# Optimization experiments

Measured on AMD Instinct MI355X. Metric: run time of the kernel, lower is better.

The kernel has to match this reference:

```python
import jax, jax.numpy as jnp
import numpy as np

D, H, E, K, N, PROJ = 512, 1024, 8, 2, 65536, 256
C = N * K // E  # expert capacity (capacity_factor=1.0 over the full token count)
LOG100 = float(np.log(100.0))


def _l2norm(v, axis=-1):
    return v / (jnp.linalg.norm(v, axis=axis, keepdims=True) + 1e-12)


def _moe(x, mask, Wp, bp, sim, temp, W1, b1, W2, b2):
    # tutel 'cosine_top' gate: cosine sim between projected tokens and expert embeddings,
    # scaled by clamped learned temperature.
    logits = _l2norm(x @ Wp + bp) @ _l2norm(sim, axis=0)
    logits = logits * jnp.exp(jnp.minimum(temp, LOG100))
    gates_all = jax.nn.softmax(logits, axis=-1)
    g, idx = jax.lax.top_k(gates_all, K)                      # [N,K]
    g = g / (jnp.sum(g, axis=-1, keepdims=True) + 1e-9)       # normalize top-k gates
    g = g * mask[:, None]                                     # zero out tokens not in this domain
    e = idx.reshape(-1)                                       # [N*K] expert id per slot
    gflat = g.reshape(-1)
    valid = jnp.repeat(mask, K)                               # [N*K]
    oh = jax.nn.one_hot(e, E, dtype=jnp.float32) * valid[:, None]
    pos = (jnp.cumsum(oh, axis=0) * oh).sum(-1).astype(jnp.int32) - 1  # slot within expert
    keep = ((pos >= 0) & (pos < C)).astype(x.dtype)           # drop overflow / masked tokens
    posc = jnp.clip(pos, 0, C - 1)
    tok = jnp.arange(N * K, dtype=jnp.int32) // K
    # dispatch -> [E,C,D]
    xd = jnp.zeros((E, C, D), x.dtype).at[e, posc].add(x[tok] * keep[:, None])
    # grouped expert FFN
    h = jax.nn.relu(jnp.einsum('ecd,edh->ech', xd, W1) + b1[:, None, :])
    y = jnp.einsum('ech,ehd->ecd', h, W2) + b2[:, None, :]
    # combine back to tokens
    out = jnp.zeros((N, D), x.dtype).at[tok].add(y[e, posc] * (gflat * keep)[:, None])
    return out


def _make_params(key):
    ks = jax.random.split(key, 4)
    Wp = jax.random.normal(ks[0], (D, PROJ), jnp.float32) * 0.02
    bp = jnp.zeros((PROJ,), jnp.float32)
    sim = jax.random.normal(ks[1], (PROJ, E), jnp.float32) * 0.02
    temp = jnp.asarray(np.log(10.0), jnp.float32)
    W1 = jax.random.normal(ks[2], (E, D, H), jnp.float32) * (1.0 / np.sqrt(D))
    b1 = jnp.zeros((E, H), jnp.float32)
    W2 = jax.random.normal(ks[3], (E, H, D), jnp.float32) * (1.0 / np.sqrt(H))
    b2 = jnp.zeros((E, D), jnp.float32)
    return Wp, bp, sim, temp, W1, b1, W2, b2


def setup_inputs():
    key = jax.random.key(0)
    kx, kl, k1, k2, k3, ksc = jax.random.split(key, 6)
    inp = {
        'x': jax.random.normal(kx, (N, D), jnp.float32),
        'domain_label': jax.random.randint(kl, (N,), 0, 2),
        'domain_scale': jax.random.normal(ksc, (1,), jnp.float32) * 0.1,
    }
    for name, k in (('sh', k1), ('day', k2), ('nt', k3)):
        Wp, bp, sim, temp, W1, b1, W2, b2 = _make_params(k)
        inp.update({name + '_Wp': Wp, name + '_bp': bp, name + '_sim': sim, name + '_temp': temp,
                    name + '_W1': W1, name + '_b1': b1, name + '_W2': W2, name + '_b2': b2})
    return inp


def reference(x, domain_label, domain_scale,
              sh_Wp, sh_bp, sh_sim, sh_temp, sh_W1, sh_b1, sh_W2, sh_b2,
              day_Wp, day_bp, day_sim, day_temp, day_W1, day_b1, day_W2, day_b2,
              nt_Wp, nt_bp, nt_sim, nt_temp, nt_W1, nt_b1, nt_W2, nt_b2):
    ones = jnp.ones((N,), jnp.float32)
    day = (domain_label == 0).astype(jnp.float32)
    night = (domain_label == 1).astype(jnp.float32)
    f_shared = _moe(x, ones, sh_Wp, sh_bp, sh_sim, sh_temp, sh_W1, sh_b1, sh_W2, sh_b2)
    f_domain = (_moe(x, day, day_Wp, day_bp, day_sim, day_temp, day_W1, day_b1, day_W2, day_b2)
                + _moe(x, night, nt_Wp, nt_bp, nt_sim, nt_temp, nt_W1, nt_b1, nt_W2, nt_b2))
    return f_shared + domain_scale * f_domain
```

## Files before the change

kernel.cpp:

```cpp
#include <hip/hip_runtime.h>

#define NTOK 65536
#define DDIM 512
#define HDIM 1024
#define NEXP 8
#define PROJ 256
#define CAP  16384
#define NSLOT (2*NTOK)
#define LOG100 4.605170185988091f

typedef __attribute__((ext_vector_type(8))) short bf16x8;
typedef __attribute__((ext_vector_type(4))) short short4v;
typedef __attribute__((ext_vector_type(4))) float f32x4;

__device__ inline float bf2f(unsigned short u){
    union { float f; unsigned int i; } c; c.i = ((unsigned int)u) << 16; return c.f;
}
__device__ inline unsigned short f2bf(float f){
    union { float f; unsigned int i; } c; c.f = f;
    unsigned int x = c.i;
    return (unsigned short)((x + 0x7fffu + ((x >> 16) & 1u)) >> 16);
}
__device__ inline void gload16(const void* g, void* lds){
    __builtin_amdgcn_global_load_lds(
        (const __attribute__((address_space(1))) unsigned int*)g,
        (__attribute__((address_space(3))) unsigned int*)lds, 16, 0, 0);
}

__global__ void init_k(const float4* __restrict__ x, ushort4* __restrict__ xb,
                       float4* __restrict__ out){
    long i = (long)blockIdx.x * 256 + threadIdx.x;
    float4 f = x[i];
    ushort4 u; u.x = f2bf(f.x); u.y = f2bf(f.y); u.z = f2bf(f.z); u.w = f2bf(f.w);
    xb[i] = u;
    out[i] = float4{0.f, 0.f, 0.f, 0.f};
}

__device__ inline void trans_body(const float* in, unsigned short* out, int R, int C){
    int rbase = blockIdx.y * 32, cbase = blockIdx.x * 32;
    if (rbase >= R || cbase >= C) return;
    __shared__ float tile[32][33];
    int tx = threadIdx.x, ty = threadIdx.y;
    #pragma unroll
    for (int i = 0; i < 4; i++)
        tile[ty + i*8][tx] = in[(long)(rbase + ty + i*8) * C + cbase + tx];
    __syncthreads();
    #pragma unroll
    for (int i = 0; i < 4; i++)
        out[(long)(cbase + ty + i*8) * R + rbase + tx] = f2bf(tile[tx][ty + i*8]);
}

__global__ __launch_bounds__(256)
void trans2_k(const float* __restrict__ W1, const float* __restrict__ W2,
              unsigned short* __restrict__ W1T, unsigned short* __restrict__ W2T)
{
    int z = blockIdx.z;
    if (z < 8) trans_body(W1 + (size_t)z*DDIM*HDIM, W1T + (size_t)z*DDIM*HDIM, DDIM, HDIM);
    else       trans_body(W2 + (size_t)(z-8)*DDIM*HDIM, W2T + (size_t)(z-8)*DDIM*HDIM, HDIM, DDIM);
}

struct W12P { const float* W1[3]; const float* W2[3]; };
__global__ __launch_bounds__(256)
void transW12all_k(W12P wp, unsigned short* __restrict__ W1T3, unsigned short* __restrict__ W2T3)
{
    int z = blockIdx.z, m = z >> 4, piece = z & 15;
    if (piece < 8)
        trans_body(wp.W1[m] + (size_t)piece*DDIM*HDIM,
                   W1T3 + ((size_t)m*8 + piece)*DDIM*HDIM, DDIM, HDIM);
    else
        trans_body(wp.W2[m] + (size_t)(piece-8)*DDIM*HDIM,
                   W2T3 + ((size_t)m*8 + piece-8)*DDIM*HDIM, HDIM, DDIM);
}

struct TpArgs { const float* Wp[3]; };
__global__ __launch_bounds__(256)
void transWp_k(TpArgs ta, unsigned short* __restrict__ WpT3)
{
    int m = blockIdx.z;
    trans_body(ta.Wp[m], WpT3 + (size_t)m*PROJ*DDIM, DDIM, PROJ);
}

struct SimArgs { const float* sim[3]; };
__global__ void simn3_k(SimArgs sa, float* __restrict__ simn3){
    __shared__ float red[256];
    const float* sim = sa.sim[blockIdx.x];
    float* simn = simn3 + (size_t)blockIdx.x * PROJ * NEXP;
    int j = threadIdx.x;
    for (int e = 0; e < NEXP; e++){
        float v = sim[j*NEXP + e];
        red[j] = v*v;
        __syncthreads();
        for (int s = 128; s > 0; s >>= 1){
            if (j < s) red[j] += red[j + s];
            __syncthreads();
        }
        float nrm = sqrtf(red[0]) + 1e-12f;
        __syncthreads();
        simn[j*NEXP + e] = v / nrm;
    }
}

struct WprodArgs { const float* Wp[3]; const float* bp[3]; };
__global__ __launch_bounds__(256)
void wprod_k(WprodArgs wa, const float* __restrict__ simn3,
             float* __restrict__ Wn3, float* __restrict__ bd3)
{
    int m = blockIdx.x;
    __shared__ float Sn[PROJ*NEXP];
    const float* Wp = wa.Wp[m];
    int t = threadIdx.x;
    for (int i = t; i < PROJ*NEXP; i += 256) Sn[i] = simn3[(size_t)m*PROJ*NEXP + i];
    __syncthreads();
    for (int r = t; r < DDIM; r += 256){
        float d[8];
        #pragma unroll
        for (int e = 0; e < 8; e++) d[e] = 0.f;
        for (int p = 0; p < PROJ; p++){
            float w = Wp[(size_t)r*PROJ + p];
            #pragma unroll
            for (int e = 0; e < 8; e++) d[e] = fmaf(w, Sn[p*8+e], d[e]);
        }
        #pragma unroll
        for (int e = 0; e < 8; e++) Wn3[((size_t)m*DDIM + r)*8 + e] = d[e];
    }
    if (t < 8){
        float s = 0.f;
        for (int p = 0; p < PROJ; p++) s = fmaf(wa.bp[m][p], Sn[p*8+t], s);
        bd3[m*8 + t] = s;
    }
}

struct PssArgs { const float* bp[3]; };
__global__ __launch_bounds__(256)
void pss_k(const unsigned short* __restrict__ WpT3, const unsigned short* __restrict__ xb,
           PssArgs pa, float* __restrict__ ssbuf)
{
    __shared__ __align__(16) short As[128*32];
    __shared__ __align__(16) short Bs[128*32];
    __shared__ float ssl[2][128];
    const int m = blockIdx.z;
    const int row0 = blockIdx.x * 128;
    const int n0 = blockIdx.y * 128;
    const unsigned short* AT = WpT3 + (size_t)m * PROJ * DDIM;
    const float* bp = pa.bp[m];

    const int t = threadIdx.x, w = t >> 6, l = t & 63;
    const int qrow = l >> 2, kc = (l & 3) * 8;
    long arowg[2], browg[2];
    #pragma unroll
    for (int q = 0; q < 2; q++){
        arowg[q] = (long)(row0 + w*32 + q*16 + qrow) * DDIM;
        browg[q] = (long)(n0   + w*32 + q*16 + qrow) * DDIM;
    }
    const int wm = (w >> 1) * 64, wn = (w & 1) * 64;
    const int fr = l & 15, fk = l >> 4;
    const int koff = fk * 8, fk4 = fk * 4;

    f32x4 acc[4][4];
    #pragma unroll
    for (int i = 0; i < 4; i++)
        #pragma unroll
        for (int j = 0; j < 4; j++) acc[i][j] = (f32x4){0.f, 0.f, 0.f, 0.f};

    for (int k0 = 0; k0 < DDIM; k0 += 32){
        __syncthreads();
        #pragma unroll
        for (int q = 0; q < 2; q++) gload16(AT + arowg[q] + k0 + kc, As + w*1024 + q*512);
        #pragma unroll
        for (int q = 0; q < 2; q++) gload16(xb + browg[q] + k0 + kc, Bs + w*1024 + q*512);
        __syncthreads();
        bf16x8 af[4], bfv[4];
        #pragma unroll
        for (int i = 0; i < 4; i++) af[i]  = *(const bf16x8*)&As[(wm + i*16 + fr)*32 + koff];
        #pragma unroll
        for (int j = 0; j < 4; j++) bfv[j] = *(const bf16x8*)&Bs[(wn + j*16 + fr)*32 + koff];
        #pragma unroll
        for (int i = 0; i < 4; i++)
            #pragma unroll
            for (int j = 0; j < 4; j++)
                acc[i][j] = __builtin_amdgcn_mfma_f32_16x16x32_bf16(af[i], bfv[j], acc[i][j], 0, 0, 0);
    }

    float part[4];
    #pragma unroll
    for (int j = 0; j < 4; j++){
        float s = 0.f;
        #pragma unroll
        for (int i = 0; i < 4; i++){
            int mc = row0 + wm + i*16 + fk4;
            float4 bb = *(const float4*)(bp + mc);
            float v0 = acc[i][j][0] + bb.x;
            float v1 = acc[i][j][1] + bb.y;
            float v2 = acc[i][j][2] + bb.z;
            float v3 = acc[i][j][3] + bb.w;
            s += v0*v0 + v1*v1 + v2*v2 + v3*v3;
        }
        s += __shfl_xor(s, 16, 64);
        s += __shfl_xor(s, 32, 64);
        part[j] = s;
    }
    if (fk == 0){
        #pragma unroll
        for (int j = 0; j < 4; j++) ssl[w >> 1][wn + j*16 + fr] = part[j];
    }
    __syncthreads();
    if (t < 128)
        ssbuf[((size_t)blockIdx.x*3 + m)*NTOK + n0 + t] = ssl[0][t] + ssl[1][t];
}

struct GfArgs { const float* tp[3]; };
__global__ __launch_bounds__(256)
void gatefin3_k(const float* __restrict__ x, const int* __restrict__ label,
                const float* __restrict__ Wn3, const float* __restrict__ bd3,
                const float* __restrict__ ssbuf, GfArgs gf,
                int* __restrict__ idx3, float* __restrict__ gw3)
{
    __shared__ float pd[3][64][26];
    const int t = threadIdx.x;
    const int tok = t & 63;
    const int qu = __builtin_amdgcn_readfirstlane(t >> 6);
    const int n = blockIdx.x * 64 + tok;

    float dots[3][8];
    #pragma unroll
    for (int m = 0; m < 3; m++)
        #pragma unroll
        for (int e = 0; e < 8; e++) dots[m][e] = 0.f;

    const float4* xp = (const float4*)(x + (size_t)n * DDIM + qu * 128);
    for (int c = 0; c < 8; c++){
        float4 xv[4];
        #pragma unroll
        for (int u = 0; u < 4; u++) xv[u] = xp[c*4 + u];
        #pragma unroll
        for (int kk = 0; kk < 16; kk++){
            float a = (kk & 2) ? ((kk & 1) ? xv[kk>>2].w : xv[kk>>2].z)
                               : ((kk & 1) ? xv[kk>>2].y : xv[kk>>2].x);
            int k = qu*128 + c*16 + kk;
            #pragma unroll
            for (int m = 0; m < 3; m++){
                const float* wr = Wn3 + ((size_t)m*DDIM + k)*8;
                float4 w0 = *(const float4*)wr;
                float4 w1 = *(const float4*)(wr + 4);
                dots[m][0] = fmaf(a, w0.x, dots[m][0]);
                dots[m][1] = fmaf(a, w0.y, dots[m][1]);
                dots[m][2] = fmaf(a, w0.z, dots[m][2]);
                dots[m][3] = fmaf(a, w0.w, dots[m][3]);
                dots[m][4] = fmaf(a, w1.x, dots[m][4]);
                dots[m][5] = fmaf(a, w1.y, dots[m][5]);
                dots[m][6] = fmaf(a, w1.z, dots[m][6]);
                dots[m][7] = fmaf(a, w1.w, dots[m][7]);
            }
        }
    }
    if (qu != 0){
        #pragma unroll
        for (int m = 0; m < 3; m++)
            #pragma unroll
            for (int e = 0; e < 8; e++) pd[qu-1][tok][m*8+e] = dots[m][e];
    }
    __syncthreads();
    if (qu == 0){
        #pragma unroll
        for (int qq = 0; qq < 3; qq++)
            #pragma unroll
            for (int m = 0; m < 3; m++)
                #pragma unroll
                for (int e = 0; e < 8; e++) dots[m][e] += pd[qq][tok][m*8+e];

        int lab = label[n];
        #pragma unroll
        for (int m = 0; m < 3; m++){
            float ss = ssbuf[(0*3+m)*(size_t)NTOK + n] + ssbuf[(1*3+m)*(size_t)NTOK + n];
            float scale = expf(fminf(gf.tp[m][0], LOG100));
            float inv = scale / (sqrtf(ss) + 1e-12f);
            float l8[8], mx = -1e30f;
            #pragma unroll
            for (int e = 0; e < 8; e++){
                l8[e] = (dots[m][e] + bd3[m*8+e]) * inv;
                mx = fmaxf(mx, l8[e]);
            }
            float g[8], s = 0.f;
            #pragma unroll
            for (int e = 0; e < 8; e++){ g[e] = expf(l8[e] - mx); s += g[e]; }
            #pragma unroll
            for (int e = 0; e < 8; e++) g[e] /= s;
            int e0 = 0; float b0 = g[0];
            #pragma unroll
            for (int e = 1; e < 8; e++) if (g[e] > b0){ b0 = g[e]; e0 = e; }
            int e1 = (e0 == 0) ? 1 : 0; float b1v = g[e1];
            #pragma unroll
            for (int e = 0; e < 8; e++) if (e != e0 && g[e] > b1v){ b1v = g[e]; e1 = e; }
            float maskv = (m == 0) ? 1.f : ((lab == m - 1) ? 1.f : 0.f);
            float s2 = b0 + b1v + 1e-9f;
            size_t base = (size_t)m * NSLOT + 2*(size_t)n;
            gw3[base]   = b0 / s2 * maskv;
            gw3[base+1] = b1v / s2 * maskv;
            idx3[base]   = e0;
            idx3[base+1] = e1;
        }
    }
}

template<int BGATHER, int OMODE>
__device__ __forceinline__
void gemm_core_t(short* As, short* Bs,
                 const unsigned short* __restrict__ AT, const unsigned short* __restrict__ Bv,
                 const float* __restrict__ bias, void* __restrict__ Cout,
                 int Kd, int Mld, int row0, int col0, int limitN,
                 const int* __restrict__ rowidx, const int* __restrict__ otok,
                 const float* __restrict__ gs)
{
    const int t = threadIdx.x;
    const int w = t >> 6, l = t & 63;
    const int qrow = l >> 2;
    const int kc = (l & 3) * 8;

    long arowg[2], browg[2];
    #pragma unroll
    for (int q = 0; q < 2; q++){
        arowg[q] = (long)(row0 + w*32 + q*16 + qrow) * Kd;
        int s = col0 + w*32 + q*16 + qrow;
        int gi = s;
        if (BGATHER) gi = (s < limitN) ? rowidx[s] : 0;
        browg[q] = (long)gi * Kd;
    }

    const int wm = (w >> 1) * 64, wn = (w & 1) * 64;
    const int fr = l & 15, fk = l >> 4;
    const int koff = fk * 8, fk4 = fk * 4;

    f32x4 acc[4][4];
    #pragma unroll
    for (int i = 0; i < 4; i++)
        #pragma unroll
        for (int j = 0; j < 4; j++) acc[i][j] = (f32x4){0.f, 0.f, 0.f, 0.f};

    for (int k0 = 0; k0 < Kd; k0 += 32){
        __syncthreads();
        #pragma unroll
        for (int q = 0; q < 2; q++) gload16(AT + arowg[q] + k0 + kc, As + w*1024 + q*512);
        #pragma unroll
        for (int q = 0; q < 2; q++) gload16(Bv + browg[q] + k0 + kc, Bs + w*1024 + q*512);
        __syncthreads();
        bf16x8 af[4], bfv[4];
        #pragma unroll
        for (int i = 0; i < 4; i++) af[i]  = *(const bf16x8*)&As[(wm + i*16 + fr)*32 + koff];
        #pragma unroll
        for (int j = 0; j < 4; j++) bfv[j] = *(const bf16x8*)&Bs[(wn + j*16 + fr)*32 + koff];
        #pragma unroll
        for (int i = 0; i < 4; i++)
            #pragma unroll
            for (int j = 0; j < 4; j++)
                acc[i][j] = __builtin_amdgcn_mfma_f32_16x16x32_bf16(af[i], bfv[j], acc[i][j], 0, 0, 0);
    }

    #pragma unroll
    for (int i = 0; i < 4; i++){
        const int mc = row0 + wm + i*16 + fk4;
        float4 bb = *(const float4*)(bias + mc);
        #pragma unroll
        for (int j = 0; j < 4; j++){
            int s = col0 + wn + j*16 + fr;
            if (s < limitN){
                if (OMODE == 1){
                    ushort4 u;
                    u.x = f2bf(fmaxf(acc[i][j][0] + bb.x, 0.f));
                    u.y = f2bf(fmaxf(acc[i][j][1] + bb.y, 0.f));
                    u.z = f2bf(fmaxf(acc[i][j][2] + bb.z, 0.f));
                    u.w = f2bf(fmaxf(acc[i][j][3] + bb.w, 0.f));
                    *(ushort4*)((unsigned short*)Cout + (long)s * Mld + mc) = u;
                } else {
                    int tk = otok[s];
                    float g = gs[s];
                    float* op = (float*)Cout + (long)tk * Mld + mc;
                    float4 c = *(const float4*)op;
                    c.x += g * (acc[i][j][0] + bb.x);
                    c.y += g * (acc[i][j][1] + bb.y);
                    c.z += g * (acc[i][j][2] + bb.z);
                    c.w += g * (acc[i][j][3] + bb.w);
                    *(float4*)op = c;
                }
            }
        }
    }
}

template<int BGATHER, int OMODE>
__device__ __forceinline__
void gemm_core_t64(short* As, short* Bs,
                   const unsigned short* __restrict__ AT, const unsigned short* __restrict__ Bv,
                   const float* __restrict__ bias, void* __restrict__ Cout,
                   int Kd, int Mld, int row0, int col0, int limitN,
                   const int* __restrict__ rowidx, const int* __restrict__ otok,
                   const float* __restrict__ gs)
{
    const int t = threadIdx.x;
    const int w = t >> 6, l = t & 63;
    const int qrow = l >> 2;
    const int seg = (l & 3) * 8;

    long arowg[2], browg[2];
    #pragma unroll
    for (int q = 0; q < 2; q++){
        arowg[q] = (long)(row0 + w*32 + q*16 + qrow) * Kd;
        int s = col0 + w*32 + q*16 + qrow;
        int gi = s;
        if (BGATHER) gi = (s < limitN) ? rowidx[s] : 0;
        browg[q] = (long)gi * Kd;
    }

    const int wm = (w >> 1) * 64, wn = (w & 1) * 64;
    const int fr = l & 15, fk = l >> 4;
    const int koff = fk * 8, fk4 = fk * 4;

    f32x4 acc[4][4];
    #pragma unroll
    for (int i = 0; i < 4; i++)
        #pragma unroll
        for (int j = 0; j < 4; j++) acc[i][j] = (f32x4){0.f, 0.f, 0.f, 0.f};

    for (int k0 = 0; k0 < Kd; k0 += 64){
        __syncthreads();
        #pragma unroll
        for (int ks = 0; ks < 2; ks++)
            #pragma unroll
            for (int q = 0; q < 2; q++)
                gload16(AT + arowg[q] + k0 + ks*32 + seg, As + ks*4096 + w*1024 + q*512);
        #pragma unroll
        for (int ks = 0; ks < 2; ks++)
            #pragma unroll
            for (int q = 0; q < 2; q++)
                gload16(Bv + browg[q] + k0 + ks*32 + seg, Bs + ks*4096 + w*1024 + q*512);
        __syncthreads();
        #pragma unroll
        for (int ks = 0; ks < 2; ks++){
            bf16x8 af[4], bfv[4];
            #pragma unroll
            for (int i = 0; i < 4; i++) af[i]  = *(const bf16x8*)&As[ks*4096 + (wm + i*16 + fr)*32 + koff];
            #pragma unroll
            for (int j = 0; j < 4; j++) bfv[j] = *(const bf16x8*)&Bs[ks*4096 + (wn + j*16 + fr)*32 + koff];
            #pragma unroll
            for (int i = 0; i < 4; i++)
                #pragma unroll
                for (int j = 0; j < 4; j++)
                    acc[i][j] = __builtin_amdgcn_mfma_f32_16x16x32_bf16(af[i], bfv[j], acc[i][j], 0, 0, 0);
        }
    }

    #pragma unroll
    for (int i = 0; i < 4; i++){
        const int mc = row0 + wm + i*16 + fk4;
        float4 bb = *(const float4*)(bias + mc);
        #pragma unroll
        for (int j = 0; j < 4; j++){
            int s = col0 + wn + j*16 + fr;
            if (s < limitN){
                if (OMODE == 1){
                    ushort4 u;
                    u.x = f2bf(fmaxf(acc[i][j][0] + bb.x, 0.f));
                    u.y = f2bf(fmaxf(acc[i][j][1] + bb.y, 0.f));
                    u.z = f2bf(fmaxf(acc[i][j][2] + bb.z, 0.f));
                    u.w = f2bf(fmaxf(acc[i][j][3] + bb.w, 0.f));
                    *(ushort4*)((unsigned short*)Cout + (long)s * Mld + mc) = u;
                } else {
                    int tk = otok[s];
                    float g = gs[s];
                    float* op = (float*)Cout + (long)tk * Mld + mc;
                    float4 c = *(const float4*)op;
                    c.x += g * (acc[i][j][0] + bb.x);
                    c.y += g * (acc[i][j][1] + bb.y);
                    c.z += g * (acc[i][j][2] + bb.z);
                    c.w += g * (acc[i][j][3] + bb.w);
                    *(float4*)op = c;
                }
            }
        }
    }
}

__device__ __forceinline__
void gemm_core_y64(short* lds,
                   const unsigned short* __restrict__ AT, const unsigned short* __restrict__ Bv,
                   const float* __restrict__ bias, float* __restrict__ out,
                   int row0, int col0, int limitN,
                   const int* __restrict__ otok, const float* __restrict__ gs)
{
    short* As = lds;
    short* Bs = lds + 4096;
    const int t = threadIdx.x, w = t >> 6, l = t & 63;
    const int seg = (l & 3) * 8;

    const long arow = (long)(row0 + w*16 + (l >> 2)) * HDIM;
    long brow[2];
    #pragma unroll
    for (int hh = 0; hh < 2; hh++)
        brow[hh] = (long)(col0 + w*32 + hh*16 + (l >> 2)) * HDIM;

    const int wm = (w >> 1) * 32, wn = (w & 1) * 64;
    const int fr = l & 15, fk = l >> 4;
    const int koff = fk * 8, fk4 = fk * 4;

    f32x4 acc[2][4];
    #pragma unroll
    for (int i = 0; i < 2; i++)
        #pragma unroll
        for (int j = 0; j < 4; j++) acc[i][j] = (f32x4){0.f, 0.f, 0.f, 0.f};

    for (int k0 = 0; k0 < HDIM; k0 += 64){
        __syncthreads();
        #pragma unroll
        for (int ks = 0; ks < 2; ks++)
            gload16(AT + arow + k0 + ks*32 + seg, As + ks*2048 + w*512);
        #pragma unroll
        for (int ks = 0; ks < 2; ks++)
            #pragma unroll
            for (int hh = 0; hh < 2; hh++)
                gload16(Bv + brow[hh] + k0 + ks*32 + seg, Bs + ks*4096 + w*1024 + hh*512);
        __syncthreads();
        #pragma unroll
        for (int ks = 0; ks < 2; ks++){
            bf16x8 af[2], bfv[4];
            #pragma unroll
            for (int i = 0; i < 2; i++)
                af[i] = *(const bf16x8*)&As[ks*2048 + (wm + i*16 + fr)*32 + koff];
            #pragma unroll
            for (int j = 0; j < 4; j++)
                bfv[j] = *(const bf16x8*)&Bs[ks*4096 + (wn + j*16 + fr)*32 + koff];
            #pragma unroll
            for (int i = 0; i < 2; i++)
                #pragma unroll
                for (int j = 0; j < 4; j++)
                    acc[i][j] = __builtin_amdgcn_mfma_f32_16x16x32_bf16(af[i], bfv[j], acc[i][j], 0, 0, 0);
        }
    }

    #pragma unroll
    for (int i = 0; i < 2; i++){
        const int mc = row0 + wm + i*16 + fk4;
        float4 bb = *(const float4*)(bias + mc);
        #pragma unroll
        for (int j = 0; j < 4; j++){
            int s = col0 + wn + j*16 + fr;
            if (s < limitN){
                int tk = otok[s];
                float g = gs[s];
                float* op = out + (long)tk * DDIM + mc;
                float4 c = *(const float4*)op;
                c.x += g * (acc[i][j][0] + bb.x);
                c.y += g * (acc[i][j][1] + bb.y);
                c.z += g * (acc[i][j][2] + bb.z);
                c.w += g * (acc[i][j][3] + bb.w);
                *(float4*)op = c;
            }
        }
    }
}

template<int BGATHER, int OMODE>
__global__ __launch_bounds__(256)
void mgemm3_k(const unsigned short* __restrict__ AT, const unsigned short* __restrict__ Bv,
              const float* __restrict__ bias, void* __restrict__ Cout,
              int Kd, int Mld,
              const int* __restrict__ rowidx, const int* __restrict__ otok,
              const float* __restrict__ gs, const int* __restrict__ cntp, int cnti)
{
    __shared__ __align__(16) short As[128*32];
    __shared__ __align__(16) short Bs[128*32];
    int limit = cntp[cnti]; if (limit > CAP) limit = CAP;
    int row0 = blockIdx.x * 128, col0 = blockIdx.y * 128;
    if (col0 >= limit) return;
    gemm_core_t<BGATHER, OMODE>(As, Bs, AT, Bv, bias, Cout, Kd, Mld,
                                row0, col0, limit, rowidx, otok, gs);
}

struct FfnP { const float* b1[3]; const float* b2[3]; };
__global__ __launch_bounds__(256)
void ffnA_k(const unsigned short* __restrict__ xb,
            const unsigned short* __restrict__ W1T3, const unsigned short* __restrict__ W2T3,
            FfnP fp, unsigned short* __restrict__ h0, unsigned short* __restrict__ h1,
            float* __restrict__ out,
            const int* __restrict__ tok3, const float* __restrict__ gslot3,
            const int* __restrict__ cntk3, int ge)
{
    __shared__ __align__(16) short lds[16384];
    const int bx = blockIdx.x, by = blockIdx.y;
    const int col0 = bx * 128;
    if (by < 8){
        if (ge >= 24) return;
        int m = ge >> 3, e = ge & 7;
        int limit = cntk3[m*16 + e]; if (limit > CAP) limit = CAP;
        if (col0 >= limit) return;
        unsigned short* hd = (ge & 1) ? h1 : h0;
        gemm_core_t64<1, 1>(lds, lds + 8192,
                            W1T3 + ((size_t)(m*8+e))*HDIM*DDIM, xb, fp.b1[m] + (size_t)e*HDIM,
                            hd, DDIM, HDIM, by*128, col0, limit,
                            tok3 + ((size_t)m*NEXP + e)*CAP, nullptr, nullptr);
    } else {
        int gy = ge - 1; if (gy < 0) return;
        int m = gy >> 3, e = gy & 7;
        int limit = cntk3[m*16 + e]; if (limit > CAP) limit = CAP;
        if (col0 >= limit) return;
        const unsigned short* hs = (gy & 1) ? h1 : h0;
        gemm_core_y64(lds, W2T3 + ((size_t)(m*8+e))*DDIM*HDIM, hs, fp.b2[m] + (size_t)e*DDIM,
                      out, (by-8)*64, col0, limit,
                      tok3 + ((size_t)m*NEXP + e)*CAP, gslot3 + ((size_t)m*NEXP + e)*CAP);
    }
}

__global__ __launch_bounds__(256)
void ffnD_k(const unsigned short* __restrict__ xb,
            const unsigned short* __restrict__ W1T3, const unsigned short* __restrict__ W2T3,
            FfnP fp, unsigned short* __restrict__ h0, unsigned short* __restrict__ h1,
            unsigned short* __restrict__ h2, unsigned short* __restrict__ h3,
            float* __restrict__ out,
            const int* __restrict__ tok3, const float* __restrict__ gslot3,
            const int* __restrict__ cntk3, int s)
{
    __shared__ __align__(16) short lds[16384];
    const int bx = blockIdx.x, by = blockIdx.y;
    const int col0 = bx * 128;
    if (by < 16){
        if (s >= 8) return;
        int m = (by < 8) ? 1 : 2;
        int g = m*NEXP + s;
        int limit = cntk3[m*16 + s]; if (limit > CAP) limit = CAP;
        if (col0 >= limit) return;
        unsigned short* hd = (m == 1) ? ((s & 1) ? h1 : h0) : ((s & 1) ? h3 : h2);
        gemm_core_t64<1, 1>(lds, lds + 8192,
                            W1T3 + (size_t)g*HDIM*DDIM, xb, fp.b1[m] + (size_t)s*HDIM,
                            hd, DDIM, HDIM, (by & 7)*128, col0, limit,
                            tok3 + (size_t)g*CAP, nullptr, nullptr);
    } else {
        int m, e; const unsigned short* hs_;
        if (s == 0){
            if (by >= 24) return;
            m = 0; e = 7; hs_ = h1;
        } else {
            m = (by < 24) ? 1 : 2;
            e = s - 1;
            hs_ = (m == 1) ? ((e & 1) ? h1 : h0) : ((e & 1) ? h3 : h2);
        }
        int g = m*NEXP + e;
        int limit = cntk3[m*16 + e]; if (limit > CAP) limit = CAP;
        if (col0 >= limit) return;
        gemm_core_y64(lds, W2T3 + (size_t)g*DDIM*HDIM, hs_, fp.b2[m] + (size_t)e*DDIM,
                      out, ((by - 16) & 7)*64, col0, limit,
                      tok3 + (size_t)g*CAP, gslot3 + (size_t)g*CAP);
    }
}

__global__ __launch_bounds__(256)
void ffnB_k(const unsigned short* __restrict__ xb,
            const unsigned short* __restrict__ W1T, const float* __restrict__ b1,
            const unsigned short* __restrict__ W2T, const float* __restrict__ b2,
            unsigned short* __restrict__ h0, unsigned short* __restrict__ h1,
            float* __restrict__ out,
            const int* __restrict__ tok, const float* __restrict__ gslot,
            const int* __restrict__ cntk, int eh)
{
    __shared__ __align__(16) short lds[12288];
    const int bx = blockIdx.x, by = blockIdx.y;
    const int col0 = bx * 128;
    if (by < 8){
        if (eh > 7) return;
        int limit = cntk[eh]; if (limit > CAP) limit = CAP;
        if (col0 >= limit) return;
        unsigned short* hd = (eh & 1) ? h1 : h0;
        gemm_core_t<1, 1>(lds, lds + 4096,
                          W1T + (size_t)eh*HDIM*DDIM, xb, b1 + (size_t)eh*HDIM,
                          hd, DDIM, HDIM, by*128, col0, limit,
                          tok + (size_t)eh*CAP, nullptr, nullptr);
    } else {
        int ey = eh - 1; if (ey < 0) return;
        int limit = cntk[ey]; if (limit > CAP) limit = CAP;
        if (col0 >= limit) return;
        const unsigned short* hs = (ey & 1) ? h1 : h0;
        gemm_core_y64(lds, W2T + (size_t)ey*DDIM*HDIM, hs, b2 + (size_t)ey*DDIM,
                      out, (by-8)*64, col0, limit,
                      tok + (size_t)ey*CAP, gslot + (size_t)ey*CAP);
    }
}

__global__ __launch_bounds__(1024)
void rank_count3_k(const int* __restrict__ idx3, const int* __restrict__ label,
                   int* __restrict__ bcnt3)
{
    __shared__ int c[NEXP];
    const int m = blockIdx.y;
    const int* idx = idx3 + (size_t)m * NSLOT;
    int t = threadIdx.x;
    if (t < NEXP) c[t] = 0;
    __syncthreads();
    int s = blockIdx.x * 1024 + t;
    int n = s >> 1;
    int e = idx[s];
    bool valid = (m == 0) || (label[n] == m - 1);
    if (valid) atomicAdd(&c[e], 1);
    __syncthreads();
    if (t < NEXP) bcnt3[((size_t)m*128 + blockIdx.x)*NEXP + t] = c[t];
}

__global__ void rank_scan3_k(const int* __restrict__ bcnt3, int* __restrict__ boff3,
                             int* __restrict__ cntk3)
{
    int m = blockIdx.x, e = threadIdx.x;
    if (e < NEXP){
        int run = 0;
        for (int b = 0; b < NSLOT/1024; b++){
            boff3[((size_t)m*128 + b)*NEXP + e] = run;
            run += bcnt3[((size_t)m*128 + b)*NEXP + e];
        }
        cntk3[m*16 + e] = run < CAP ? run : CAP;
    }
}

__global__ __launch_bounds__(1024)
void rank_assign3_k(const int* __restrict__ idx3, const int* __restrict__ label,
                    const int* __restrict__ boff3, const float* __restrict__ gw3,
                    const float* __restrict__ dscale,
                    int* __restrict__ tok3, float* __restrict__ gs3)
{
    __shared__ int wcnt[16][NEXP];
    __shared__ int woff[16][NEXP];
    const int m = blockIdx.y;
    const int* idx = idx3 + (size_t)m * NSLOT;
    const float* gw = gw3 + (size_t)m * NSLOT;
    int t = threadIdx.x;
    int s = blockIdx.x * 1024 + t;
    int n = s >> 1;
    int e = idx[s];
    bool valid = (m == 0) || (label[n] == m - 1);
    int w = t >> 6, lane = t & 63;
    unsigned long long lt = (lane == 0) ? 0ull : ((1ull << lane) - 1ull);
    int myrank = 0;
    #pragma unroll
    for (int ei = 0; ei < NEXP; ei++){
        unsigned long long bal = __ballot(valid && (e == ei));
        if (ei == e) myrank = __popcll(bal & lt);
        if (lane == 0) wcnt[w][ei] = __popcll(bal);
    }
    __syncthreads();
    if (t < NEXP){
        int run = boff3[((size_t)m*128 + blockIdx.x)*NEXP + t];
        for (int w2 = 0; w2 < 16; w2++){
            woff[w2][t] = run;
            run += wcnt[w2][t];
        }
    }
    __syncthreads();
    int pos = woff[w][e] + myrank;
    bool keep = valid && (pos < CAP);
    if (keep){
        float scale = (m > 0) ? dscale[0] : 1.f;
        tok3[((size_t)m*NEXP + e)*CAP + pos] = n;
        gs3[((size_t)m*NEXP + e)*CAP + pos] = gw[s] * scale;
    }
}

extern "C" void kernel_launch(void* const* d_in, const int* in_sizes, int n_in,
                              void* d_out, int out_size, void* d_ws, size_t ws_size,
                              hipStream_t stream)
{
    (void)in_sizes; (void)n_in; (void)out_size;
    const float* x      = (const float*)d_in[0];
    const int*   label  = (const int*)  d_in[1];
    const float* dscale = (const float*)d_in[2];
    float* out = (float*)d_out;

    const size_t XB  = (size_t)NTOK * DDIM * 2;
    const size_t HS  = (size_t)CAP * HDIM * 2;
    const size_t WPT = (size_t)3 * PROJ * DDIM * 2;
    const size_t SS  = (size_t)2 * 3 * NTOK * 4;
    const size_t WN  = (size_t)3 * DDIM * 8 * 4;
    const size_t SMALL = WPT + SS + WN + 256 +
                         (size_t)3*PROJ*NEXP*4 +
                         (size_t)3*NSLOT*4*2 +
                         (size_t)3*NEXP*CAP*4*2 +
                         (size_t)3*128*NEXP*4*2 + 256;
    const size_t W12A = (size_t)2 * 3 * NEXP * DDIM * HDIM * 2;
    const size_t W12B = (size_t)2 * NEXP * DDIM * HDIM * 2;
    const size_t common = XB + HS + SMALL;

    int tier;
    if      (ws_size >= common + 3*HS + W12A) tier = 0;
    else if (ws_size >= common + HS + W12A)   tier = 1;
    else if (ws_size >= common + HS + W12B)   tier = 2;
    else if (ws_size >= common + W12B)        tier = 3;
    else return;

    char* p = (char*)d_ws;
    unsigned short* xb   = (unsigned short*)p; p += XB;
    unsigned short* h0   = (unsigned short*)p; p += HS;
    unsigned short* WpT3 = (unsigned short*)p; p += WPT;
    float* ssbuf = (float*)p;  p += SS;
    float* Wn3   = (float*)p;  p += WN;
    float* bd3   = (float*)p;  p += 256;
    float* simn3 = (float*)p;  p += (size_t)3*PROJ*NEXP*4;
    int*   idx3  = (int*)p;    p += (size_t)3*NSLOT*4;
    float* gw3   = (float*)p;  p += (size_t)3*NSLOT*4;
    int*   tok3  = (int*)p;    p += (size_t)3*NEXP*CAP*4;
    float* gslot3= (float*)p;  p += (size_t)3*NEXP*CAP*4;
    int*   bcnt3 = (int*)p;    p += (size_t)3*128*NEXP*4;
    int*   boff3 = (int*)p;    p += (size_t)3*128*NEXP*4;
    int*   cntk3 = (int*)p;    p += 256;
    unsigned short* h1 = nullptr;
    unsigned short* h2 = nullptr;
    unsigned short* h3 = nullptr;
    if (tier <= 2){ h1 = (unsigned short*)p; p += HS; }
    if (tier == 0){ h2 = (unsigned short*)p; p += HS; h3 = (unsigned short*)p; p += HS; }
    unsigned short* Wbuf = (unsigned short*)p;

    SimArgs sa; TpArgs ta; WprodArgs wa; PssArgs pa; GfArgs gf; W12P wp; FfnP fp;
    for (int m = 0; m < 3; m++){
        ta.Wp[m] = (const float*)d_in[3 + 8*m + 0];
        wa.Wp[m] = ta.Wp[m];
        wa.bp[m] = (const float*)d_in[3 + 8*m + 1];
        pa.bp[m] = wa.bp[m];
        sa.sim[m] = (const float*)d_in[3 + 8*m + 2];
        gf.tp[m] = (const float*)d_in[3 + 8*m + 3];
        wp.W1[m] = (const float*)d_in[3 + 8*m + 4];
        fp.b1[m] = (const float*)d_in[3 + 8*m + 5];
        wp.W2[m] = (const float*)d_in[3 + 8*m + 6];
        fp.b2[m] = (const float*)d_in[3 + 8*m + 7];
    }

    init_k<<<dim3(NTOK*DDIM/4/256), dim3(256), 0, stream>>>(
        (const float4*)x, (ushort4*)xb, (float4*)out);
    simn3_k<<<dim3(3), dim3(256), 0, stream>>>(sa, simn3);
    transWp_k<<<dim3(PROJ/32, DDIM/32, 3), dim3(32,8), 0, stream>>>(ta, WpT3);
    wprod_k<<<dim3(3), dim3(256), 0, stream>>>(wa, simn3, Wn3, bd3);
    pss_k<<<dim3(2, NTOK/128, 3), dim3(256), 0, stream>>>(WpT3, xb, pa, ssbuf);
    gatefin3_k<<<dim3(NTOK/64), dim3(256), 0, stream>>>(
        x, label, Wn3, bd3, ssbuf, gf, idx3, gw3);

    rank_count3_k<<<dim3(NSLOT/1024, 3), dim3(1024), 0, stream>>>(idx3, label, bcnt3);
    rank_scan3_k<<<dim3(3), dim3(64), 0, stream>>>(bcnt3, boff3, cntk3);
    rank_assign3_k<<<dim3(NSLOT/1024, 3), dim3(1024), 0, stream>>>(
        idx3, label, boff3, gw3, dscale, tok3, gslot3);

    if (tier <= 1){
        unsigned short* W1T3 = Wbuf;
        unsigned short* W2T3 = Wbuf + (size_t)3*NEXP*DDIM*HDIM;
        transW12all_k<<<dim3(32, 32, 48), dim3(32,8), 0, stream>>>(wp, W1T3, W2T3);
        if (tier == 0){
            for (int ge = 0; ge < 8; ge++)
                ffnA_k<<<dim3(128, 16), 256, 0, stream>>>(
                    xb, W1T3, W2T3, fp, h0, h1, out, tok3, gslot3, cntk3, ge);
            for (int s = 0; s <= 8; s++)
                ffnD_k<<<dim3(128, 32), 256, 0, stream>>>(
                    xb, W1T3, W2T3, fp, h0, h1, h2, h3, out, tok3, gslot3, cntk3, s);
        } else {
            for (int ge = 0; ge <= 24; ge++)
                ffnA_k<<<dim3(128, 16), 256, 0, stream>>>(
                    xb, W1T3, W2T3, fp, h0, h1, out, tok3, gslot3, cntk3, ge);
        }
    } else {
        unsigned short* W1T = Wbuf;
        unsigned short* W2T = Wbuf + (size_t)NEXP*DDIM*HDIM;
        for (int m = 0; m < 3; m++){
            trans2_k<<<dim3(32, 32, 16), dim3(32,8), 0, stream>>>(wp.W1[m], wp.W2[m], W1T, W2T);
            const int* tokm = tok3 + (size_t)m*NEXP*CAP;
            const float* gsm = gslot3 + (size_t)m*NEXP*CAP;
            const int* cntm = cntk3 + m*16;
            if (tier == 2){
                for (int eh = 0; eh <= 8; eh++)
                    ffnB_k<<<dim3(128, 16), 256, 0, stream>>>(
                        xb, W1T, fp.b1[m], W2T, fp.b2[m], h0, h1, out, tokm, gsm, cntm, eh);
            } else {
                for (int e = 0; e < NEXP; e++){
                    mgemm3_k<1, 1><<<dim3(HDIM/128, CAP/128), 256, 0, stream>>>(
                        W1T + (size_t)e*HDIM*DDIM, xb, fp.b1[m] + (size_t)e*HDIM, h0,
                        DDIM, HDIM, tokm + (size_t)e*CAP, nullptr, nullptr, cntm, e);
                    mgemm3_k<0, 3><<<dim3(DDIM/128, CAP/128), 256, 0, stream>>>(
                        W2T + (size_t)e*DDIM*HDIM, h0, fp.b2[m] + (size_t)e*DDIM, out,
                        HDIM, DDIM, nullptr, tokm + (size_t)e*CAP, gsm + (size_t)e*CAP, cntm, e);
                }
            }
        }
    }
}
```

Before: 1.686 ms.

## Double-buffer LDS tiles in expert FFN GEMMs to overlap loads with MFMA

Both expert GEMM cores now use a two-stage LDS ping-pong with a K step of 32. The next K-slice's global-to-LDS loads are issued before the MFMAs on the current slice, and only one barrier is kept per step. The aim is to hide global load latency behind matrix math instead of stalling at a load barrier every step. The cost is twice as many loop iterations and barriers, and the ffnB kernel's LDS grows, which may reduce occupancy.

```diff
diff --git a/kernel.cpp b/kernel.cpp
--- a/kernel.cpp
+++ b/kernel.cpp
@@ -388,17 +388,17 @@
 
 template<int BGATHER, int OMODE>
 __device__ __forceinline__
-void gemm_core_t64(short* As, short* Bs,
-                   const unsigned short* __restrict__ AT, const unsigned short* __restrict__ Bv,
-                   const float* __restrict__ bias, void* __restrict__ Cout,
-                   int Kd, int Mld, int row0, int col0, int limitN,
-                   const int* __restrict__ rowidx, const int* __restrict__ otok,
-                   const float* __restrict__ gs)
+void gemm_core_t2(short* lds,
+                  const unsigned short* __restrict__ AT, const unsigned short* __restrict__ Bv,
+                  const float* __restrict__ bias, void* __restrict__ Cout,
+                  int Kd, int Mld, int row0, int col0, int limitN,
+                  const int* __restrict__ rowidx, const int* __restrict__ otok,
+                  const float* __restrict__ gs)
 {
     const int t = threadIdx.x;
     const int w = t >> 6, l = t & 63;
     const int qrow = l >> 2;
-    const int seg = (l & 3) * 8;
+    const int kc = (l & 3) * 8;
 
     long arowg[2], browg[2];
     #pragma unroll
@@ -420,32 +420,38 @@
         #pragma unroll
         for (int j = 0; j < 4; j++) acc[i][j] = (f32x4){0.f, 0.f, 0.f, 0.f};
 
-    for (int k0 = 0; k0 < Kd; k0 += 64){
+    const int nsteps = Kd >> 5;
+    #pragma unroll
+    for (int q = 0; q < 2; q++) gload16(AT + arowg[q] + kc, lds + w*1024 + q*512);
+    #pragma unroll
+    for (int q = 0; q < 2; q++) gload16(Bv + browg[q] + kc, lds + 8192 + w*1024 + q*512);
+    __syncthreads();
+
+    for (int s = 0; s < nsteps; s++){
+        const int cur = s & 1;
+        if (s + 1 < nsteps){
+            const int nxt = cur ^ 1;
+            const int k = (s + 1) << 5;
+            short* An = lds + nxt*4096;
+            short* Bn = lds + 8192 + nxt*4096;
+            #pragma unroll
+            for (int q = 0; q < 2; q++) gload16(AT + arowg[q] + k + kc, An + w*1024 + q*512);
+            #pragma unroll
+            for (int q = 0; q < 2; q++) gload16(Bv + browg[q] + k + kc, Bn + w*1024 + q*512);
+        }
+        short* Ac = lds + cur*4096;
+        short* Bc = lds + 8192 + cur*4096;
+        bf16x8 af[4], bfv[4];
+        #pragma unroll
+        for (int i = 0; i < 4; i++) af[i]  = *(const bf16x8*)&Ac[(wm + i*16 + fr)*32 + koff];
+        #pragma unroll
+        for (int j = 0; j < 4; j++) bfv[j] = *(const bf16x8*)&Bc[(wn + j*16 + fr)*32 + koff];
+        #pragma unroll
+        for (int i = 0; i < 4; i++)
+            #pragma unroll
+            for (int j = 0; j < 4; j++)
+                acc[i][j] = __builtin_amdgcn_mfma_f32_16x16x32_bf16(af[i], bfv[j], acc[i][j], 0, 0, 0);
         __syncthreads();
-        #pragma unroll
-        for (int ks = 0; ks < 2; ks++)
-            #pragma unroll
-            for (int q = 0; q < 2; q++)
-                gload16(AT + arowg[q] + k0 + ks*32 + seg, As + ks*4096 + w*1024 + q*512);
-        #pragma unroll
-        for (int ks = 0; ks < 2; ks++)
-            #pragma unroll
-            for (int q = 0; q < 2; q++)
-                gload16(Bv + browg[q] + k0 + ks*32 + seg, Bs + ks*4096 + w*1024 + q*512);
-        __syncthreads();
-        #pragma unroll
-        for (int ks = 0; ks < 2; ks++){
-            bf16x8 af[4], bfv[4];
-            #pragma unroll
-            for (int i = 0; i < 4; i++) af[i]  = *(const bf16x8*)&As[ks*4096 + (wm + i*16 + fr)*32 + koff];
-            #pragma unroll
-            for (int j = 0; j < 4; j++) bfv[j] = *(const bf16x8*)&Bs[ks*4096 + (wn + j*16 + fr)*32 + koff];
-            #pragma unroll
-            for (int i = 0; i < 4; i++)
-                #pragma unroll
-                for (int j = 0; j < 4; j++)
-                    acc[i][j] = __builtin_amdgcn_mfma_f32_16x16x32_bf16(af[i], bfv[j], acc[i][j], 0, 0, 0);
-        }
     }
 
     #pragma unroll
@@ -480,14 +486,12 @@
 }
 
 __device__ __forceinline__
-void gemm_core_y64(short* lds,
-                   const unsigned short* __restrict__ AT, const unsigned short* __restrict__ Bv,
-                   const float* __restrict__ bias, float* __restrict__ out,
-                   int row0, int col0, int limitN,
-                   const int* __restrict__ otok, const float* __restrict__ gs)
-{
-    short* As = lds;
-    short* Bs = lds + 4096;
+void gemm_core_y2(short* lds,
+                  const unsigned short* __restrict__ AT, const unsigned short* __restrict__ Bv,
+                  const float* __restrict__ bias, float* __restrict__ out,
+                  int row0, int col0, int limitN,
+                  const int* __restrict__ otok, const float* __restrict__ gs)
+{
     const int t = threadIdx.x, w = t >> 6, l = t & 63;
     const int seg = (l & 3) * 8;
 
@@ -507,32 +511,38 @@
         #pragma unroll
         for (int j = 0; j < 4; j++) acc[i][j] = (f32x4){0.f, 0.f, 0.f, 0.f};
 
-    for (int k0 = 0; k0 < HDIM; k0 += 64){
+    const int nsteps = HDIM >> 5;
+    gload16(AT + arow + seg, lds + w*512);
+    #pragma unroll
+    for (int hh = 0; hh < 2; hh++)
+        gload16(Bv + brow[hh] + seg, lds + 4096 + w*1024 + hh*512);
+    __syncthreads();
+
+    for (int s = 0; s < nsteps; s++){
+        const int cur = s & 1;
+        if (s + 1 < nsteps){
+            const int nxt = cur ^ 1;
+            const int k = (s + 1) << 5;
+            gload16(AT + arow + k + seg, lds + nxt*2048 + w*512);
+            #pragma unroll
+            for (int hh = 0; hh < 2; hh++)
+                gload16(Bv + brow[hh] + k + seg, lds + 4096 + nxt*4096 + w*1024 + hh*512);
+        }
+        short* Ac = lds + cur*2048;
+        short* Bc = lds + 4096 + cur*4096;
+        bf16x8 af[2], bfv[4];
+        #pragma unroll
+        for (int i = 0; i < 2; i++)
+            af[i] = *(const bf16x8*)&Ac[(wm + i*16 + fr)*32 + koff];
+        #pragma unroll
+        for (int j = 0; j < 4; j++)
+            bfv[j] = *(const bf16x8*)&Bc[(wn + j*16 + fr)*32 + koff];
+        #pragma unroll
+        for (int i = 0; i < 2; i++)
+            #pragma unroll
+            for (int j = 0; j < 4; j++)
+                acc[i][j] = __builtin_amdgcn_mfma_f32_16x16x32_bf16(af[i], bfv[j], acc[i][j], 0, 0, 0);
         __syncthreads();
-        #pragma unroll
-        for (int ks = 0; ks < 2; ks++)
-            gload16(AT + arow + k0 + ks*32 + seg, As + ks*2048 + w*512);
-        #pragma unroll
-        for (int ks = 0; ks < 2; ks++)
-            #pragma unroll
-            for (int hh = 0; hh < 2; hh++)
-                gload16(Bv + brow[hh] + k0 + ks*32 + seg, Bs + ks*4096 + w*1024 + hh*512);
-        __syncthreads();
-        #pragma unroll
-        for (int ks = 0; ks < 2; ks++){
-            bf16x8 af[2], bfv[4];
-            #pragma unroll
-            for (int i = 0; i < 2; i++)
-                af[i] = *(const bf16x8*)&As[ks*2048 + (wm + i*16 + fr)*32 + koff];
-            #pragma unroll
-            for (int j = 0; j < 4; j++)
-                bfv[j] = *(const bf16x8*)&Bs[ks*4096 + (wn + j*16 + fr)*32 + koff];
-            #pragma unroll
-            for (int i = 0; i < 2; i++)
-                #pragma unroll
-                for (int j = 0; j < 4; j++)
-                    acc[i][j] = __builtin_amdgcn_mfma_f32_16x16x32_bf16(af[i], bfv[j], acc[i][j], 0, 0, 0);
-        }
     }
 
     #pragma unroll
@@ -592,19 +602,19 @@
         int limit = cntk3[m*16 + e]; if (limit > CAP) limit = CAP;
         if (col0 >= limit) return;
         unsigned short* hd = (ge & 1) ? h1 : h0;
-        gemm_core_t64<1, 1>(lds, lds + 8192,
-                            W1T3 + ((size_t)(m*8+e))*HDIM*DDIM, xb, fp.b1[m] + (size_t)e*HDIM,
-                            hd, DDIM, HDIM, by*128, col0, limit,
-                            tok3 + ((size_t)m*NEXP + e)*CAP, nullptr, nullptr);
+        gemm_core_t2<1, 1>(lds,
+                           W1T3 + ((size_t)(m*8+e))*HDIM*DDIM, xb, fp.b1[m] + (size_t)e*HDIM,
+                           hd, DDIM, HDIM, by*128, col0, limit,
+                           tok3 + ((size_t)m*NEXP + e)*CAP, nullptr, nullptr);
     } else {
         int gy = ge - 1; if (gy < 0) return;
         int m = gy >> 3, e = gy & 7;
         int limit = cntk3[m*16 + e]; if (limit > CAP) limit = CAP;
         if (col0 >= limit) return;
         const unsigned short* hs = (gy & 1) ? h1 : h0;
-        gemm_core_y64(lds, W2T3 + ((size_t)(m*8+e))*DDIM*HDIM, hs, fp.b2[m] + (size_t)e*DDIM,
-                      out, (by-8)*64, col0, limit,
-                      tok3 + ((size_t)m*NEXP + e)*CAP, gslot3 + ((size_t)m*NEXP + e)*CAP);
+        gemm_core_y2(lds, W2T3 + ((size_t)(m*8+e))*DDIM*HDIM, hs, fp.b2[m] + (size_t)e*DDIM,
+                     out, (by-8)*64, col0, limit,
+                     tok3 + ((size_t)m*NEXP + e)*CAP, gslot3 + ((size_t)m*NEXP + e)*CAP);
     }
 }
 
@@ -627,10 +637,10 @@
         int limit = cntk3[m*16 + s]; if (limit > CAP) limit = CAP;
         if (col0 >= limit) return;
         unsigned short* hd = (m == 1) ? ((s & 1) ? h1 : h0) : ((s & 1) ? h3 : h2);
-        gemm_core_t64<1, 1>(lds, lds + 8192,
-                            W1T3 + (size_t)g*HDIM*DDIM, xb, fp.b1[m] + (size_t)s*HDIM,
-                            hd, DDIM, HDIM, (by & 7)*128, col0, limit,
-                            tok3 + (size_t)g*CAP, nullptr, nullptr);
+        gemm_core_t2<1, 1>(lds,
+                           W1T3 + (size_t)g*HDIM*DDIM, xb, fp.b1[m] + (size_t)s*HDIM,
+                           hd, DDIM, HDIM, (by & 7)*128, col0, limit,
+                           tok3 + (size_t)g*CAP, nullptr, nullptr);
     } else {
         int m, e; const unsigned short* hs_;
         if (s == 0){
@@ -644,9 +654,9 @@
         int g = m*NEXP + e;
         int limit = cntk3[m*16 + e]; if (limit > CAP) limit = CAP;
         if (col0 >= limit) return;
-        gemm_core_y64(lds, W2T3 + (size_t)g*DDIM*HDIM, hs_, fp.b2[m] + (size_t)e*DDIM,
-                      out, ((by - 16) & 7)*64, col0, limit,
-                      tok3 + (size_t)g*CAP, gslot3 + (size_t)g*CAP);
+        gemm_core_y2(lds, W2T3 + (size_t)g*DDIM*HDIM, hs_, fp.b2[m] + (size_t)e*DDIM,
+                     out, ((by - 16) & 7)*64, col0, limit,
+                     tok3 + (size_t)g*CAP, gslot3 + (size_t)g*CAP);
     }
 }
 
@@ -659,7 +669,7 @@
             const int* __restrict__ tok, const float* __restrict__ gslot,
             const int* __restrict__ cntk, int eh)
 {
-    __shared__ __align__(16) short lds[12288];
+    __shared__ __align__(16) short lds[16384];
     const int bx = blockIdx.x, by = blockIdx.y;
     const int col0 = bx * 128;
     if (by < 8){
@@ -667,18 +677,18 @@
         int limit = cntk[eh]; if (limit > CAP) limit = CAP;
         if (col0 >= limit) return;
         unsigned short* hd = (eh & 1) ? h1 : h0;
-        gemm_core_t<1, 1>(lds, lds + 4096,
-                          W1T + (size_t)eh*HDIM*DDIM, xb, b1 + (size_t)eh*HDIM,
-                          hd, DDIM, HDIM, by*128, col0, limit,
-                          tok + (size_t)eh*CAP, nullptr, nullptr);
+        gemm_core_t2<1, 1>(lds,
+                           W1T + (size_t)eh*HDIM*DDIM, xb, b1 + (size_t)eh*HDIM,
+                           hd, DDIM, HDIM, by*128, col0, limit,
+                           tok + (size_t)eh*CAP, nullptr, nullptr);
     } else {
         int ey = eh - 1; if (ey < 0) return;
         int limit = cntk[ey]; if (limit > CAP) limit = CAP;
         if (col0 >= limit) return;
         const unsigned short* hs = (ey & 1) ? h1 : h0;
-        gemm_core_y64(lds, W2T + (size_t)ey*DDIM*HDIM, hs, b2 + (size_t)ey*DDIM,
-                      out, (by-8)*64, col0, limit,
-                      tok + (size_t)ey*CAP, gslot + (size_t)ey*CAP);
+        gemm_core_y2(lds, W2T + (size_t)ey*DDIM*HDIM, hs, b2 + (size_t)ey*DDIM,
+                     out, (by-8)*64, col0, limit,
+                     tok + (size_t)ey*CAP, gslot + (size_t)ey*CAP);
     }
 }
 
```

Measured after the change: 1.739 ms. 1.03x slower.
